# Kernel optimization log

Hardware: AMD Instinct MI355X
Metric: run time of the kernel (lower is better)

The kernel has to match this reference:

```python
import jax, jax.numpy as jnp
import numpy as np

ALPHA = 0.1
THETA = 0.5
LAYERS = 4
N, E, D_IN, H, D_OUT = 100000, 1600000, 128, 128, 128


def setup_inputs() -> dict:
    key = jax.random.key(0)
    ks = jax.random.split(key, 9)
    x = jax.random.normal(ks[0], (N, D_IN), jnp.float32)
    edge_src = jax.random.randint(ks[1], (E,), 0, N, jnp.int32)
    edge_dst = jax.random.randint(ks[2], (E,), 0, N, jnp.int32)
    edge_w = jax.random.uniform(ks[3], (E,), jnp.float32)
    s_in = 1.0 / np.sqrt(D_IN)
    s_h = 1.0 / np.sqrt(H)
    W0 = jax.random.uniform(ks[4], (D_IN, H), jnp.float32, -s_in, s_in)
    b0 = jax.random.uniform(ks[5], (H,), jnp.float32, -s_in, s_in)
    W1 = jax.random.uniform(ks[6], (H, D_OUT), jnp.float32, -s_h, s_h)
    b1 = jax.random.uniform(ks[7], (D_OUT,), jnp.float32, -s_h, s_h)
    glorot = np.sqrt(6.0 / (H + H))
    convW = jax.random.uniform(ks[8], (LAYERS, H, H), jnp.float32, -glorot, glorot)
    return dict(x=x, edge_src=edge_src, edge_dst=edge_dst, edge_w=edge_w,
                W0=W0, b0=b0, W1=W1, b1=b1, convW=convW)


def reference(x, edge_src, edge_dst, edge_w, W0, b0, W1, b1, convW):
    # input projection + relu; x_0 is the initial residual (GCNII)
    h = jax.nn.relu(x @ W0 + b0)
    x0 = h
    for l in range(LAYERS):
        beta = float(np.log(THETA / (l + 1) + 1.0))
        # SpMM: agg[i] = sum_{(j->i) in E} w_e * h[j]
        msg = h[edge_src] * edge_w[:, None]                      # [E, H]
        agg = jax.ops.segment_sum(msg, edge_dst, num_segments=N)  # [N, H]
        out = (1.0 - ALPHA) * agg + ALPHA * x0                    # initial residual
        out = (1.0 - beta) * out + beta * (out @ convW[l])        # identity mapping
        h = jax.nn.relu(out)
    logits = h @ W1 + b1
    return jax.nn.log_softmax(logits, axis=-1)
```

## Files before the change

kernel.cpp:

```cpp
#include <hip/hip_runtime.h>
#include <math.h>

typedef unsigned int uint;
typedef unsigned short ushort;
using bf8   = __attribute__((ext_vector_type(8))) short;
using f32x4 = __attribute__((ext_vector_type(4))) float;

__device__ inline ushort f2bf(float f) {
  uint u = __float_as_uint(f);
  return (ushort)((u + 0x7fffu + ((u >> 16) & 1u)) >> 16);
}
__device__ inline float bf2f(ushort s) { return __uint_as_float(((uint)s) << 16); }
__device__ inline uint packbf2(float a, float b) {
  uint ua = __float_as_uint(a), ub = __float_as_uint(b);
  ua = (ua + 0x7fffu + ((ua >> 16) & 1u)) >> 16;
  ub = (ub + 0x7fffu + ((ub >> 16) & 1u)) & 0xffff0000u;
  return ua | ub;
}
__device__ inline float bflo(uint u) { return __uint_as_float(u << 16); }
__device__ inline float bfhi(uint u) { return __uint_as_float(u & 0xffff0000u); }

__global__ void hist_k(const int* __restrict__ dst, int* __restrict__ cnt, int E) {
  int tid = blockIdx.x * blockDim.x + threadIdx.x;
  int stride4 = gridDim.x * blockDim.x * 4;
  for (int base = tid * 4; base + 3 < E; base += stride4) {
    int4 d = *(const int4*)&dst[base];
    atomicAdd(&cnt[d.x], 1);
    atomicAdd(&cnt[d.y], 1);
    atomicAdd(&cnt[d.z], 1);
    atomicAdd(&cnt[d.w], 1);
  }
  int tail0 = (E & ~3);
  int e = tail0 + tid;
  if (e < E) atomicAdd(&cnt[dst[e]], 1);
}

__global__ __launch_bounds__(256) void scanA_k(const int* __restrict__ cnt,
                                               int* __restrict__ bsum, int N) {
  __shared__ int red[256];
  int tid = threadIdx.x;
  int i0 = blockIdx.x * 1024 + tid * 4;
  int s = 0;
  #pragma unroll
  for (int k = 0; k < 4; ++k) { int i = i0 + k; if (i < N) s += cnt[i]; }
  red[tid] = s;
  __syncthreads();
  for (int off = 128; off; off >>= 1) {
    if (tid < off) red[tid] += red[tid + off];
    __syncthreads();
  }
  if (tid == 0) bsum[blockIdx.x] = red[0];
}

__global__ __launch_bounds__(128) void scanB_k(const int* __restrict__ bsum,
                                               int* __restrict__ bbase, int nb) {
  __shared__ int buf[2][128];
  int tid = threadIdx.x;
  buf[0][tid] = (tid < nb) ? bsum[tid] : 0;
  __syncthreads();
  int pin = 0;
  for (int off = 1; off < 128; off <<= 1) {
    int x = buf[pin][tid];
    if (tid >= off) x += buf[pin][tid - off];
    buf[1 - pin][tid] = x;
    __syncthreads();
    pin = 1 - pin;
  }
  if (tid < nb) bbase[tid] = (tid == 0) ? 0 : buf[pin][tid - 1];
}

__global__ __launch_bounds__(256) void scanC_k(const int* __restrict__ cnt,
    const int* __restrict__ bbase, int* __restrict__ rp, int N, int E) {
  __shared__ int buf[2][256];
  int tid = threadIdx.x;
  int i0 = blockIdx.x * 1024 + tid * 4;
  int c[4]; int s = 0;
  #pragma unroll
  for (int k = 0; k < 4; ++k) { int i = i0 + k; c[k] = (i < N) ? cnt[i] : 0; s += c[k]; }
  buf[0][tid] = s;
  __syncthreads();
  int pin = 0;
  for (int off = 1; off < 256; off <<= 1) {
    int x = buf[pin][tid];
    if (tid >= off) x += buf[pin][tid - off];
    buf[1 - pin][tid] = x;
    __syncthreads();
    pin = 1 - pin;
  }
  int run = bbase[blockIdx.x] + buf[pin][tid] - s;
  #pragma unroll
  for (int k = 0; k < 4; ++k) {
    int i = i0 + k;
    if (i < N) { rp[i] = run; run += c[k]; }
  }
  if (blockIdx.x == 0 && tid == 0) rp[N] = E;
}

__global__ void scatter_k(const int* __restrict__ src, const int* __restrict__ dst,
                          const float* __restrict__ w, const int* __restrict__ rp,
                          int* __restrict__ cnt, int2* __restrict__ epk, int E) {
  int stride = gridDim.x * blockDim.x;
  for (int e = blockIdx.x * blockDim.x + threadIdx.x; e < E; e += stride) {
    int d = dst[e];
    int off = atomicAdd(&cnt[d], -1) - 1;
    epk[rp[d] + off] = make_int2(src[e], __float_as_int(w[e]));
  }
}

__global__ __launch_bounds__(256) void spmm_k(const int* __restrict__ rp,
    const int2* __restrict__ epk, const ushort* __restrict__ hbf,
    const ushort* __restrict__ x0bf, ushort* __restrict__ outbf, int N) {
  int gw = (blockIdx.x * blockDim.x + threadIdx.x) >> 6;
  int lane = threadIdx.x & 63;
  if (gw >= N) return;
  int grp = lane >> 4, l16 = lane & 15;
  int b = __builtin_amdgcn_readfirstlane(rp[gw]);
  int e = __builtin_amdgcn_readfirstlane(rp[gw + 1]);
  float a0 = 0.f, a1 = 0.f, a2 = 0.f, a3 = 0.f;
  float a4 = 0.f, a5 = 0.f, a6 = 0.f, a7 = 0.f;
  const uint* hb = (const uint*)hbf;
  int j = b + grp;
  for (; j + 12 < e; j += 16) {
    int2 e0 = epk[j], e1 = epk[j + 4], e2 = epk[j + 8], e3 = epk[j + 12];
    float w0 = __int_as_float(e0.y), w1 = __int_as_float(e1.y);
    float w2 = __int_as_float(e2.y), w3 = __int_as_float(e3.y);
    uint4 h0 = ((const uint4*)hb)[(size_t)e0.x * 16 + l16];
    uint4 h1 = ((const uint4*)hb)[(size_t)e1.x * 16 + l16];
    uint4 h2 = ((const uint4*)hb)[(size_t)e2.x * 16 + l16];
    uint4 h3 = ((const uint4*)hb)[(size_t)e3.x * 16 + l16];
    a0 = fmaf(w0, bflo(h0.x), a0); a1 = fmaf(w0, bfhi(h0.x), a1);
    a2 = fmaf(w0, bflo(h0.y), a2); a3 = fmaf(w0, bfhi(h0.y), a3);
    a4 = fmaf(w0, bflo(h0.z), a4); a5 = fmaf(w0, bfhi(h0.z), a5);
    a6 = fmaf(w0, bflo(h0.w), a6); a7 = fmaf(w0, bfhi(h0.w), a7);
    a0 = fmaf(w1, bflo(h1.x), a0); a1 = fmaf(w1, bfhi(h1.x), a1);
    a2 = fmaf(w1, bflo(h1.y), a2); a3 = fmaf(w1, bfhi(h1.y), a3);
    a4 = fmaf(w1, bflo(h1.z), a4); a5 = fmaf(w1, bfhi(h1.z), a5);
    a6 = fmaf(w1, bflo(h1.w), a6); a7 = fmaf(w1, bfhi(h1.w), a7);
    a0 = fmaf(w2, bflo(h2.x), a0); a1 = fmaf(w2, bfhi(h2.x), a1);
    a2 = fmaf(w2, bflo(h2.y), a2); a3 = fmaf(w2, bfhi(h2.y), a3);
    a4 = fmaf(w2, bflo(h2.z), a4); a5 = fmaf(w2, bfhi(h2.z), a5);
    a6 = fmaf(w2, bflo(h2.w), a6); a7 = fmaf(w2, bfhi(h2.w), a7);
    a0 = fmaf(w3, bflo(h3.x), a0); a1 = fmaf(w3, bfhi(h3.x), a1);
    a2 = fmaf(w3, bflo(h3.y), a2); a3 = fmaf(w3, bfhi(h3.y), a3);
    a4 = fmaf(w3, bflo(h3.z), a4); a5 = fmaf(w3, bfhi(h3.z), a5);
    a6 = fmaf(w3, bflo(h3.w), a6); a7 = fmaf(w3, bfhi(h3.w), a7);
  }
  for (; j + 4 < e; j += 8) {
    int2 e0 = epk[j], e1 = epk[j + 4];
    float w0 = __int_as_float(e0.y), w1 = __int_as_float(e1.y);
    uint4 h0 = ((const uint4*)hb)[(size_t)e0.x * 16 + l16];
    uint4 h1 = ((const uint4*)hb)[(size_t)e1.x * 16 + l16];
    a0 = fmaf(w0, bflo(h0.x), a0); a1 = fmaf(w0, bfhi(h0.x), a1);
    a2 = fmaf(w0, bflo(h0.y), a2); a3 = fmaf(w0, bfhi(h0.y), a3);
    a4 = fmaf(w0, bflo(h0.z), a4); a5 = fmaf(w0, bfhi(h0.z), a5);
    a6 = fmaf(w0, bflo(h0.w), a6); a7 = fmaf(w0, bfhi(h0.w), a7);
    a0 = fmaf(w1, bflo(h1.x), a0); a1 = fmaf(w1, bfhi(h1.x), a1);
    a2 = fmaf(w1, bflo(h1.y), a2); a3 = fmaf(w1, bfhi(h1.y), a3);
    a4 = fmaf(w1, bflo(h1.z), a4); a5 = fmaf(w1, bfhi(h1.z), a5);
    a6 = fmaf(w1, bflo(h1.w), a6); a7 = fmaf(w1, bfhi(h1.w), a7);
  }
  for (; j < e; j += 4) {
    int2 e0 = epk[j];
    float w0 = __int_as_float(e0.y);
    uint4 h0 = ((const uint4*)hb)[(size_t)e0.x * 16 + l16];
    a0 = fmaf(w0, bflo(h0.x), a0); a1 = fmaf(w0, bfhi(h0.x), a1);
    a2 = fmaf(w0, bflo(h0.y), a2); a3 = fmaf(w0, bfhi(h0.y), a3);
    a4 = fmaf(w0, bflo(h0.z), a4); a5 = fmaf(w0, bfhi(h0.z), a5);
    a6 = fmaf(w0, bflo(h0.w), a6); a7 = fmaf(w0, bfhi(h0.w), a7);
  }
  a0 += __shfl_xor(a0, 16); a1 += __shfl_xor(a1, 16);
  a2 += __shfl_xor(a2, 16); a3 += __shfl_xor(a3, 16);
  a4 += __shfl_xor(a4, 16); a5 += __shfl_xor(a5, 16);
  a6 += __shfl_xor(a6, 16); a7 += __shfl_xor(a7, 16);
  a0 += __shfl_xor(a0, 32); a1 += __shfl_xor(a1, 32);
  a2 += __shfl_xor(a2, 32); a3 += __shfl_xor(a3, 32);
  a4 += __shfl_xor(a4, 32); a5 += __shfl_xor(a5, 32);
  a6 += __shfl_xor(a6, 32); a7 += __shfl_xor(a7, 32);
  if (grp == 0) {
    uint4 xv = ((const uint4*)x0bf)[(size_t)gw * 16 + l16];
    float o0 = 0.9f * a0 + 0.1f * bflo(xv.x);
    float o1 = 0.9f * a1 + 0.1f * bfhi(xv.x);
    float o2 = 0.9f * a2 + 0.1f * bflo(xv.y);
    float o3 = 0.9f * a3 + 0.1f * bfhi(xv.y);
    float o4 = 0.9f * a4 + 0.1f * bflo(xv.z);
    float o5 = 0.9f * a5 + 0.1f * bfhi(xv.z);
    float o6 = 0.9f * a6 + 0.1f * bflo(xv.w);
    float o7 = 0.9f * a7 + 0.1f * bfhi(xv.w);
    uint4 u;
    u.x = packbf2(o0, o1); u.y = packbf2(o2, o3);
    u.z = packbf2(o4, o5); u.w = packbf2(o6, o7);
    ((uint4*)outbf)[(size_t)gw * 16 + l16] = u;
  }
}

template<int MODE, int ABF>
__global__ __launch_bounds__(256, 4) void gemm_mfma(const void* __restrict__ inv,
    const float* __restrict__ W, const float* __restrict__ bias,
    float* __restrict__ outf, ushort* __restrict__ outbf, ushort* __restrict__ outbf2,
    float cin, float cw, int N) {
  __shared__ ushort Wt[128][136];
  const float*  inf = (const float*)inv;
  const ushort* inb = (const ushort*)inv;
  int tid = threadIdx.x;

  for (int i = tid; i < 128 * 32; i += 256) {
    int k = i >> 5, n4 = (i & 31) << 2;
    float4 v = *(const float4*)&W[(size_t)k * 128 + n4];
    Wt[n4 + 0][k] = f2bf(v.x);
    Wt[n4 + 1][k] = f2bf(v.y);
    Wt[n4 + 2][k] = f2bf(v.z);
    Wt[n4 + 3][k] = f2bf(v.w);
  }
  __syncthreads();

  int w = tid >> 6, lane = tid & 63;
  int l15 = lane & 15, hi = lane >> 4;
  int rbase = blockIdx.x * 128 + w * 32;

  f32x4 acc[2][8];
  #pragma unroll
  for (int mi = 0; mi < 2; ++mi)
    #pragma unroll
    for (int ni = 0; ni < 8; ++ni)
      acc[mi][ni] = (f32x4){0.f, 0.f, 0.f, 0.f};

  int r0 = min(rbase + l15, N - 1);
  int r1 = min(rbase + 16 + l15, N - 1);

  #pragma unroll
  for (int kt = 0; kt < 4; ++kt) {
    int koff = kt * 32 + hi * 8;
    bf8 a0, a1;
    if (ABF) {
      a0 = *(const bf8*)&inb[(size_t)r0 * 128 + koff];
      a1 = *(const bf8*)&inb[(size_t)r1 * 128 + koff];
    } else {
      float4 f0 = *(const float4*)&inf[(size_t)r0 * 128 + koff];
      float4 f1 = *(const float4*)&inf[(size_t)r0 * 128 + koff + 4];
      float4 g0 = *(const float4*)&inf[(size_t)r1 * 128 + koff];
      float4 g1 = *(const float4*)&inf[(size_t)r1 * 128 + koff + 4];
      union { bf8 v; uint u[4]; } ta, tb;
      ta.u[0] = packbf2(f0.x, f0.y); ta.u[1] = packbf2(f0.z, f0.w);
      ta.u[2] = packbf2(f1.x, f1.y); ta.u[3] = packbf2(f1.z, f1.w);
      tb.u[0] = packbf2(g0.x, g0.y); tb.u[1] = packbf2(g0.z, g0.w);
      tb.u[2] = packbf2(g1.x, g1.y); tb.u[3] = packbf2(g1.z, g1.w);
      a0 = ta.v; a1 = tb.v;
    }
    #pragma unroll
    for (int ni = 0; ni < 8; ++ni) {
      bf8 b = *(const bf8*)&Wt[ni * 16 + l15][koff];
      acc[0][ni] = __builtin_amdgcn_mfma_f32_16x16x32_bf16(a0, b, acc[0][ni], 0, 0, 0);
      acc[1][ni] = __builtin_amdgcn_mfma_f32_16x16x32_bf16(a1, b, acc[1][ni], 0, 0, 0);
    }
  }

  float bcol[8];
  if (MODE != 1) {
    #pragma unroll
    for (int ni = 0; ni < 8; ++ni) bcol[ni] = bias[ni * 16 + l15];
  }

  #pragma unroll
  for (int mi = 0; mi < 2; ++mi) {
    #pragma unroll
    for (int reg = 0; reg < 4; ++reg) {
      int row = rbase + mi * 16 + 4 * hi + reg;
      bool valid = (row < N);
      float y[8];
      #pragma unroll
      for (int ni = 0; ni < 8; ++ni) y[ni] = acc[mi][ni][reg];
      if (MODE == 1) {
        if (valid) {
          #pragma unroll
          for (int ni = 0; ni < 8; ++ni) {
            float iv = bf2f(inb[(size_t)row * 128 + ni * 16 + l15]);
            y[ni] = fmaxf(cin * iv + cw * y[ni], 0.f);
          }
        }
      } else {
        #pragma unroll
        for (int ni = 0; ni < 8; ++ni) y[ni] += bcol[ni];
        if (MODE == 0) {
          #pragma unroll
          for (int ni = 0; ni < 8; ++ni) y[ni] = fmaxf(y[ni], 0.f);
        }
      }
      if (MODE == 2) {
        float m = y[0];
        #pragma unroll
        for (int ni = 1; ni < 8; ++ni) m = fmaxf(m, y[ni]);
        #pragma unroll
        for (int off = 1; off <= 8; off <<= 1) m = fmaxf(m, __shfl_xor(m, off));
        float s = 0.f;
        #pragma unroll
        for (int ni = 0; ni < 8; ++ni) s += expf(y[ni] - m);
        #pragma unroll
        for (int off = 1; off <= 8; off <<= 1) s += __shfl_xor(s, off);
        float lg = m + logf(s);
        #pragma unroll
        for (int ni = 0; ni < 8; ++ni) y[ni] -= lg;
      }
      if (valid) {
        if (MODE == 2) {
          #pragma unroll
          for (int ni = 0; ni < 8; ++ni)
            outf[(size_t)row * 128 + ni * 16 + l15] = y[ni];
        } else {
          #pragma unroll
          for (int ni = 0; ni < 8; ++ni) {
            ushort u = f2bf(y[ni]);
            outbf[(size_t)row * 128 + ni * 16 + l15] = u;
            if (MODE == 0) outbf2[(size_t)row * 128 + ni * 16 + l15] = u;
          }
        }
      }
    }
  }
}

extern "C" void kernel_launch(void* const* d_in, const int* in_sizes, int n_in,
                              void* d_out, int out_size, void* d_ws, size_t ws_size,
                              hipStream_t stream) {
  const float* x     = (const float*)d_in[0];
  const int*   esrc  = (const int*)d_in[1];
  const int*   edst  = (const int*)d_in[2];
  const float* ew    = (const float*)d_in[3];
  const float* W0    = (const float*)d_in[4];
  const float* b0    = (const float*)d_in[5];
  const float* W1    = (const float*)d_in[6];
  const float* b1    = (const float*)d_in[7];
  const float* convW = (const float*)d_in[8];
  int N = in_sizes[0] / 128;
  int E = in_sizes[1];
  float* outp = (float*)d_out;

  char* ws = (char*)d_ws;
  size_t off = 0;
  auto alloc = [&](size_t bytes) {
    void* p = ws + off;
    off += (bytes + 255) & ~(size_t)255;
    return p;
  };
  ushort* hbf   = (ushort*)alloc((size_t)N * 128 * 2);
  ushort* x0bf  = (ushort*)alloc((size_t)N * 128 * 2);
  ushort* bufB  = (ushort*)alloc((size_t)N * 128 * 2);
  ushort* bufA  = (ushort*)alloc((size_t)N * 128 * 2);
  int*    rp    = (int*)alloc((size_t)(N + 1) * 4);
  int*    cnt   = (int*)alloc((size_t)N * 4);
  int2*   epk   = (int2*)alloc((size_t)E * 8);
  int nbScan = (N + 1023) / 1024;
  int*    bsum  = (int*)alloc((size_t)nbScan * 4);
  int*    bbase = (int*)alloc((size_t)nbScan * 4);

  hipMemsetAsync(cnt, 0, (size_t)N * 4, stream);
  hist_k<<<2048, 256, 0, stream>>>(edst, cnt, E);
  scanA_k<<<nbScan, 256, 0, stream>>>(cnt, bsum, N);
  scanB_k<<<1, 128, 0, stream>>>(bsum, bbase, nbScan);
  scanC_k<<<nbScan, 256, 0, stream>>>(cnt, bbase, rp, N, E);
  scatter_k<<<2048, 256, 0, stream>>>(esrc, edst, ew, rp, cnt, epk, E);

  int gemmBlocks = (N + 127) / 128;
  int spmmBlocks = (N + 3) / 4;

  gemm_mfma<0, 0><<<gemmBlocks, 256, 0, stream>>>(x, W0, b0, nullptr, hbf, x0bf, 0.f, 1.f, N);

  for (int l = 0; l < 4; ++l) {
    float beta = logf(0.5f / (float)(l + 1) + 1.f);
    spmm_k<<<spmmBlocks, 256, 0, stream>>>(rp, epk, hbf, x0bf, bufB, N);
    gemm_mfma<1, 1><<<gemmBlocks, 256, 0, stream>>>(
        bufB, convW + (size_t)l * 128 * 128, nullptr,
        nullptr, (l == 3) ? bufA : hbf, nullptr,
        1.f - beta, beta, N);
  }

  gemm_mfma<2, 1><<<gemmBlocks, 256, 0, stream>>>(bufA, W1, b1, outp, nullptr, nullptr, 0.f, 1.f, N);
}
```

Before: 596.0 us.

## Assign one node per 16-lane group in SpMM instead of one per wave

The SpMM kernel now maps each 16-lane group to a separate destination node rather than splitting one node's edges across four groups of a wave. This removes the cross-group shuffle reduction and the idle lanes during the epilogue, and gives each group a longer sequential edge loop. The trade-off is divergence within a wave when the four nodes have different degrees, and row pointers are no longer wave-uniform scalar loads.

```diff
diff --git a/kernel.cpp b/kernel.cpp
--- a/kernel.cpp
+++ b/kernel.cpp
@@ -110,24 +110,22 @@
 __global__ __launch_bounds__(256) void spmm_k(const int* __restrict__ rp,
     const int2* __restrict__ epk, const ushort* __restrict__ hbf,
     const ushort* __restrict__ x0bf, ushort* __restrict__ outbf, int N) {
-  int gw = (blockIdx.x * blockDim.x + threadIdx.x) >> 6;
-  int lane = threadIdx.x & 63;
-  if (gw >= N) return;
-  int grp = lane >> 4, l16 = lane & 15;
-  int b = __builtin_amdgcn_readfirstlane(rp[gw]);
-  int e = __builtin_amdgcn_readfirstlane(rp[gw + 1]);
+  int node = (blockIdx.x * blockDim.x + threadIdx.x) >> 4;
+  int l16 = threadIdx.x & 15;
+  if (node >= N) return;
+  int b = rp[node], e = rp[node + 1];
   float a0 = 0.f, a1 = 0.f, a2 = 0.f, a3 = 0.f;
   float a4 = 0.f, a5 = 0.f, a6 = 0.f, a7 = 0.f;
-  const uint* hb = (const uint*)hbf;
-  int j = b + grp;
-  for (; j + 12 < e; j += 16) {
-    int2 e0 = epk[j], e1 = epk[j + 4], e2 = epk[j + 8], e3 = epk[j + 12];
+  const uint4* hb4 = (const uint4*)hbf;
+  int j = b;
+  for (; j + 3 < e; j += 4) {
+    int2 e0 = epk[j], e1 = epk[j + 1], e2 = epk[j + 2], e3 = epk[j + 3];
     float w0 = __int_as_float(e0.y), w1 = __int_as_float(e1.y);
     float w2 = __int_as_float(e2.y), w3 = __int_as_float(e3.y);
-    uint4 h0 = ((const uint4*)hb)[(size_t)e0.x * 16 + l16];
-    uint4 h1 = ((const uint4*)hb)[(size_t)e1.x * 16 + l16];
-    uint4 h2 = ((const uint4*)hb)[(size_t)e2.x * 16 + l16];
-    uint4 h3 = ((const uint4*)hb)[(size_t)e3.x * 16 + l16];
+    uint4 h0 = hb4[(size_t)e0.x * 16 + l16];
+    uint4 h1 = hb4[(size_t)e1.x * 16 + l16];
+    uint4 h2 = hb4[(size_t)e2.x * 16 + l16];
+    uint4 h3 = hb4[(size_t)e3.x * 16 + l16];
     a0 = fmaf(w0, bflo(h0.x), a0); a1 = fmaf(w0, bfhi(h0.x), a1);
     a2 = fmaf(w0, bflo(h0.y), a2); a3 = fmaf(w0, bfhi(h0.y), a3);
     a4 = fmaf(w0, bflo(h0.z), a4); a5 = fmaf(w0, bfhi(h0.z), a5);
@@ -145,52 +143,28 @@
     a4 = fmaf(w3, bflo(h3.z), a4); a5 = fmaf(w3, bfhi(h3.z), a5);
     a6 = fmaf(w3, bflo(h3.w), a6); a7 = fmaf(w3, bfhi(h3.w), a7);
   }
-  for (; j + 4 < e; j += 8) {
-    int2 e0 = epk[j], e1 = epk[j + 4];
-    float w0 = __int_as_float(e0.y), w1 = __int_as_float(e1.y);
-    uint4 h0 = ((const uint4*)hb)[(size_t)e0.x * 16 + l16];
-    uint4 h1 = ((const uint4*)hb)[(size_t)e1.x * 16 + l16];
+  for (; j < e; ++j) {
+    int2 e0 = epk[j];
+    float w0 = __int_as_float(e0.y);
+    uint4 h0 = hb4[(size_t)e0.x * 16 + l16];
     a0 = fmaf(w0, bflo(h0.x), a0); a1 = fmaf(w0, bfhi(h0.x), a1);
     a2 = fmaf(w0, bflo(h0.y), a2); a3 = fmaf(w0, bfhi(h0.y), a3);
     a4 = fmaf(w0, bflo(h0.z), a4); a5 = fmaf(w0, bfhi(h0.z), a5);
     a6 = fmaf(w0, bflo(h0.w), a6); a7 = fmaf(w0, bfhi(h0.w), a7);
-    a0 = fmaf(w1, bflo(h1.x), a0); a1 = fmaf(w1, bfhi(h1.x), a1);
-    a2 = fmaf(w1, bflo(h1.y), a2); a3 = fmaf(w1, bfhi(h1.y), a3);
-    a4 = fmaf(w1, bflo(h1.z), a4); a5 = fmaf(w1, bfhi(h1.z), a5);
-    a6 = fmaf(w1, bflo(h1.w), a6); a7 = fmaf(w1, bfhi(h1.w), a7);
-  }
-  for (; j < e; j += 4) {
-    int2 e0 = epk[j];
-    float w0 = __int_as_float(e0.y);
-    uint4 h0 = ((const uint4*)hb)[(size_t)e0.x * 16 + l16];
-    a0 = fmaf(w0, bflo(h0.x), a0); a1 = fmaf(w0, bfhi(h0.x), a1);
-    a2 = fmaf(w0, bflo(h0.y), a2); a3 = fmaf(w0, bfhi(h0.y), a3);
-    a4 = fmaf(w0, bflo(h0.z), a4); a5 = fmaf(w0, bfhi(h0.z), a5);
-    a6 = fmaf(w0, bflo(h0.w), a6); a7 = fmaf(w0, bfhi(h0.w), a7);
-  }
-  a0 += __shfl_xor(a0, 16); a1 += __shfl_xor(a1, 16);
-  a2 += __shfl_xor(a2, 16); a3 += __shfl_xor(a3, 16);
-  a4 += __shfl_xor(a4, 16); a5 += __shfl_xor(a5, 16);
-  a6 += __shfl_xor(a6, 16); a7 += __shfl_xor(a7, 16);
-  a0 += __shfl_xor(a0, 32); a1 += __shfl_xor(a1, 32);
-  a2 += __shfl_xor(a2, 32); a3 += __shfl_xor(a3, 32);
-  a4 += __shfl_xor(a4, 32); a5 += __shfl_xor(a5, 32);
-  a6 += __shfl_xor(a6, 32); a7 += __shfl_xor(a7, 32);
-  if (grp == 0) {
-    uint4 xv = ((const uint4*)x0bf)[(size_t)gw * 16 + l16];
-    float o0 = 0.9f * a0 + 0.1f * bflo(xv.x);
-    float o1 = 0.9f * a1 + 0.1f * bfhi(xv.x);
-    float o2 = 0.9f * a2 + 0.1f * bflo(xv.y);
-    float o3 = 0.9f * a3 + 0.1f * bfhi(xv.y);
-    float o4 = 0.9f * a4 + 0.1f * bflo(xv.z);
-    float o5 = 0.9f * a5 + 0.1f * bfhi(xv.z);
-    float o6 = 0.9f * a6 + 0.1f * bflo(xv.w);
-    float o7 = 0.9f * a7 + 0.1f * bfhi(xv.w);
-    uint4 u;
-    u.x = packbf2(o0, o1); u.y = packbf2(o2, o3);
-    u.z = packbf2(o4, o5); u.w = packbf2(o6, o7);
-    ((uint4*)outbf)[(size_t)gw * 16 + l16] = u;
-  }
+  }
+  uint4 xv = ((const uint4*)x0bf)[(size_t)node * 16 + l16];
+  float o0 = 0.9f * a0 + 0.1f * bflo(xv.x);
+  float o1 = 0.9f * a1 + 0.1f * bfhi(xv.x);
+  float o2 = 0.9f * a2 + 0.1f * bflo(xv.y);
+  float o3 = 0.9f * a3 + 0.1f * bfhi(xv.y);
+  float o4 = 0.9f * a4 + 0.1f * bflo(xv.z);
+  float o5 = 0.9f * a5 + 0.1f * bfhi(xv.z);
+  float o6 = 0.9f * a6 + 0.1f * bflo(xv.w);
+  float o7 = 0.9f * a7 + 0.1f * bfhi(xv.w);
+  uint4 u;
+  u.x = packbf2(o0, o1); u.y = packbf2(o2, o3);
+  u.z = packbf2(o4, o5); u.w = packbf2(o6, o7);
+  ((uint4*)outbf)[(size_t)node * 16 + l16] = u;
 }
 
 template<int MODE, int ABF>
@@ -360,7 +334,7 @@
   scatter_k<<<2048, 256, 0, stream>>>(esrc, edst, ew, rp, cnt, epk, E);
 
   int gemmBlocks = (N + 127) / 128;
-  int spmmBlocks = (N + 3) / 4;
+  int spmmBlocks = (N + 15) / 16;
 
   gemm_mfma<0, 0><<<gemmBlocks, 256, 0, stream>>>(x, W0, b0, nullptr, hbf, x0bf, 0.f, 1.f, N);
 
```

New measurement: 582.6 us. -2.2%, faster.
